# Kernel optimization log

Hardware: AMD Instinct MI355X
Metric: run time of the kernel (lower is better)

## Reference

```python
import jax, jax.numpy as jnp
import numpy as np

SCALE = 100.0          # sigmoid sharpness used as soft comparator in long division
PRECISION_BITS = 16    # number of long-division iterations (ReciprocalFFN layers)


def setup_inputs() -> dict:
    key = jax.random.key(0)
    kq, kk, kv = jax.random.split(key, 3)
    B, D, N = 8192, 1024, 2048
    return {
        "query": jax.random.normal(kq, (B, D), dtype=jnp.float32),
        "keys": jax.random.normal(kk, (N, D), dtype=jnp.float32),
        "values": jax.random.normal(kv, (N, D), dtype=jnp.float32),
    }


def _reciprocal_scan(divisor):
    """16-step non-restoring long division computing ~1/divisor.

    Mirrors ReciprocalFFN: state = (remainder, quotient), remainder starts at 1,
    each step: doubled = 2*r; step = sigmoid(SCALE*(doubled - d));
    r' = doubled - d*step; q' = q + 2^{-(i+1)} * step.
    divisor: (B, 1) -> returns quotient (B, 1).
    """
    bit_weights = 2.0 ** -(jnp.arange(PRECISION_BITS, dtype=jnp.float32) + 1.0)

    def body(carry, w):
        r, q = carry
        doubled = r * 2.0
        step = jax.nn.sigmoid(SCALE * (doubled - divisor))
        return (doubled - divisor * step, q + w * step), None

    init = (jnp.ones_like(divisor), jnp.zeros_like(divisor))
    (_, quotient), _ = jax.lax.scan(body, init, bit_weights)
    return quotient


def reference(query, keys, values):
    # Baked-mode forward: QK scores -> softmax1 with FFN long-division reciprocal
    # -> weighted sum of values.
    scale = keys.shape[-1] ** -0.5
    scores = jnp.einsum("bd,nd->bn", query, keys) * scale          # (B, N)
    exps = jnp.exp(scores - jnp.max(scores, axis=-1, keepdims=True))
    sum_exp = 1.0 + jnp.sum(exps, axis=-1, keepdims=True)           # (B, 1)
    reciprocal = _reciprocal_scan(sum_exp)                          # (B, 1)
    weights = exps * reciprocal                                     # (B, N)
    return jnp.einsum("bn,nd->bd", weights, values)                 # (B, D)
```

## Files before the change

### kernel.cpp

```cpp
#include <hip/hip_runtime.h>
#include <hip/hip_bf16.h>
#include <stdint.h>

#define BQ   8192
#define DIM  1024
#define NK   2048

typedef unsigned short u16;
using f32x4  = __attribute__((ext_vector_type(4))) float;
using bf16x8 = __attribute__((ext_vector_type(8))) __bf16;
using f16x8  = __attribute__((ext_vector_type(8))) _Float16;
using u16x4  = __attribute__((ext_vector_type(4))) unsigned short;
using u16x8  = __attribute__((ext_vector_type(8))) unsigned short;


__device__ __forceinline__ u16 f2bf(float f) {
    uint32_t u = __float_as_uint(f);
    u += 0x7FFFu + ((u >> 16) & 1u);
    return (u16)(u >> 16);
}

__device__ __forceinline__ u16 f2h(float f) {
    _Float16 h = (_Float16)f;
    return __builtin_bit_cast(unsigned short, h);
}

__device__ __forceinline__ void gload_lds16(const void* g, void* l) {
    __builtin_amdgcn_global_load_lds(
        (const __attribute__((address_space(1))) void*)g,
        (__attribute__((address_space(3))) void*)l,
        16, 0, 0);
}

template<bool F16>
__device__ __forceinline__ f32x4 mfmaT(u16x8 a, u16x8 b, f32x4 c) {
    if constexpr (F16)
        return __builtin_amdgcn_mfma_f32_16x16x32_f16(
            __builtin_bit_cast(f16x8, a), __builtin_bit_cast(f16x8, b), c, 0, 0, 0);
    else
        return __builtin_amdgcn_mfma_f32_16x16x32_bf16(
            __builtin_bit_cast(bf16x8, a), __builtin_bit_cast(bf16x8, b), c, 0, 0, 0);
}


__global__ void cvt_f32_bf16(const float* __restrict__ in, u16* __restrict__ out, int n4) {
    int i = blockIdx.x * blockDim.x + threadIdx.x;
    if (i < n4) {
        f32x4 v = reinterpret_cast<const f32x4*>(in)[i];
        u16x4 o;
        o.x = f2bf(v[0]); o.y = f2bf(v[1]); o.z = f2bf(v[2]); o.w = f2bf(v[3]);
        reinterpret_cast<u16x4*>(out)[i] = o;
    }
}

__global__ void transpose_cvt(const float* __restrict__ V, u16* __restrict__ VT) {
    __shared__ float tile[32][33];
    int d0 = blockIdx.x * 32;
    int n0 = blockIdx.y * 32;
    int tx = threadIdx.x, ty = threadIdx.y;
#pragma unroll
    for (int i = 0; i < 4; ++i)
        tile[ty + i * 8][tx] = V[(size_t)(n0 + ty + i * 8) * DIM + d0 + tx];
    __syncthreads();
#pragma unroll
    for (int i = 0; i < 4; ++i)
        VT[(size_t)(d0 + ty + i * 8) * NK + n0 + tx] = f2h(tile[tx][ty + i * 8]);
}


template<int BN, bool F16, typename OT>
__global__ __launch_bounds__(512, 2)
void gemm256(const u16* __restrict__ A, const u16* __restrict__ B, OT* __restrict__ C,
             int K, int lda, int ldb, int ldc, float scale, int nbn) {
    constexpr int WTN  = BN / 4;
    constexpr int NREP = BN / 64;
    constexpr int NH   = NREP / 2;
    constexpr int BCALLS = (BN == 256) ? 4 : 2;

    __shared__ u16 As[2][256 * 64];
    __shared__ u16 Bs[2][BN * 64];

    const int tid  = threadIdx.x;
    const int wave = tid >> 6;
    const int lane = tid & 63;
    const int wr = wave >> 2;
    const int wc = wave & 3;

    int id = blockIdx.x;
    const int cpx = gridDim.x >> 3;
    id = (id & 7) * cpx + (id >> 3);
    const int bm = id / nbn;
    const int bn = id % nbn;

    const int lsub  = lane >> 3;
    const int lslot = lane & 7;
    const int srcColEl = ((lslot ^ lsub) << 3);

    const int aRow0 = wr * 128 + wc * 32;
    int bRow0;
    if constexpr (BN == 256) bRow0 = (wc >> 1) * 128 + (wr * 2 + (wc & 1)) * 32;
    else                     bRow0 = wave * 16;

    const u16* aSrc = A + (size_t)(bm * 256 + aRow0 + lsub) * lda + srcColEl;
    const u16* bSrc = B + (size_t)(bn * BN  + bRow0 + lsub) * ldb + srcColEl;

    f32x4 acc[8][NREP] = {};

    const int NT = K >> 6;

    auto STAGE = [&](int buf, int kt) {
        const size_t ko = (size_t)kt * 64;
#pragma unroll
        for (int c2 = 0; c2 < 4; ++c2)
            gload_lds16(aSrc + (size_t)c2 * 8 * lda + ko, &As[buf][(aRow0 + c2 * 8) * 64]);
#pragma unroll
        for (int c2 = 0; c2 < BCALLS; ++c2)
            gload_lds16(bSrc + (size_t)c2 * 8 * ldb + ko, &Bs[buf][(bRow0 + c2 * 8) * 64]);
    };

    auto LDA_frag = [&](const char* base, int m, int kk) -> u16x8 {
        int r   = wr * 128 + m * 16 + (lane & 15);
        int off = r * 128 + (((kk * 64) + ((lane >> 4) << 4)) ^ ((lane & 7) << 4));
        return *reinterpret_cast<const u16x8*>(base + off);
    };
    auto LDB_frag = [&](const char* base, int n, int kk) -> u16x8 {
        int r   = wc * WTN + n * 16 + (lane & 15);
        int off = r * 128 + (((kk * 64) + ((lane >> 4) << 4)) ^ ((lane & 7) << 4));
        return *reinterpret_cast<const u16x8*>(base + off);
    };

    STAGE(0, 0);
    __syncthreads();

    int cbuf = 0;
    for (int t = 0; t < NT; ++t) {
        if (t + 1 < NT) STAGE(cbuf ^ 1, t + 1);
        __builtin_amdgcn_sched_barrier(0);

        const char* aB = (const char*)&As[cbuf][0];
        const char* bB = (const char*)&Bs[cbuf][0];

        u16x8 af[4][2];
        u16x8 bf0[NH][2], bf1[NH][2];

#pragma unroll
        for (int mi = 0; mi < 4; ++mi) { af[mi][0] = LDA_frag(aB, mi, 0); af[mi][1] = LDA_frag(aB, mi, 1); }
#pragma unroll
        for (int ni = 0; ni < NH; ++ni) { bf0[ni][0] = LDB_frag(bB, ni, 0); bf0[ni][1] = LDB_frag(bB, ni, 1); }
        __builtin_amdgcn_s_setprio(1);
#pragma unroll
        for (int mi = 0; mi < 4; ++mi)
#pragma unroll
            for (int ni = 0; ni < NH; ++ni) {
                acc[mi][ni] = mfmaT<F16>(af[mi][0], bf0[ni][0], acc[mi][ni]);
                acc[mi][ni] = mfmaT<F16>(af[mi][1], bf0[ni][1], acc[mi][ni]);
            }
        __builtin_amdgcn_s_setprio(0);

#pragma unroll
        for (int ni = 0; ni < NH; ++ni) { bf1[ni][0] = LDB_frag(bB, NH + ni, 0); bf1[ni][1] = LDB_frag(bB, NH + ni, 1); }
        __builtin_amdgcn_s_setprio(1);
#pragma unroll
        for (int mi = 0; mi < 4; ++mi)
#pragma unroll
            for (int ni = 0; ni < NH; ++ni) {
                acc[mi][NH + ni] = mfmaT<F16>(af[mi][0], bf1[ni][0], acc[mi][NH + ni]);
                acc[mi][NH + ni] = mfmaT<F16>(af[mi][1], bf1[ni][1], acc[mi][NH + ni]);
            }
        __builtin_amdgcn_s_setprio(0);

#pragma unroll
        for (int mi = 0; mi < 4; ++mi) { af[mi][0] = LDA_frag(aB, 4 + mi, 0); af[mi][1] = LDA_frag(aB, 4 + mi, 1); }
        __builtin_amdgcn_s_setprio(1);
#pragma unroll
        for (int mi = 0; mi < 4; ++mi)
#pragma unroll
            for (int ni = 0; ni < NH; ++ni) {
                acc[4 + mi][NH + ni] = mfmaT<F16>(af[mi][0], bf1[ni][0], acc[4 + mi][NH + ni]);
                acc[4 + mi][NH + ni] = mfmaT<F16>(af[mi][1], bf1[ni][1], acc[4 + mi][NH + ni]);
            }
        __builtin_amdgcn_s_setprio(0);

        __builtin_amdgcn_s_setprio(1);
#pragma unroll
        for (int mi = 0; mi < 4; ++mi)
#pragma unroll
            for (int ni = 0; ni < NH; ++ni) {
                acc[4 + mi][ni] = mfmaT<F16>(af[mi][0], bf0[ni][0], acc[4 + mi][ni]);
                acc[4 + mi][ni] = mfmaT<F16>(af[mi][1], bf0[ni][1], acc[4 + mi][ni]);
            }
        __builtin_amdgcn_s_setprio(0);

        __syncthreads();
        cbuf ^= 1;
    }

    const int col0 = bn * BN + wc * WTN + (lane & 15);
    const int row0 = bm * 256 + wr * 128 + ((lane >> 4) << 2);
#pragma unroll
    for (int m = 0; m < 8; ++m) {
#pragma unroll
        for (int j = 0; j < 4; ++j) {
            int row = row0 + m * 16 + j;
            OT* cp = C + (size_t)row * ldc + col0;
#pragma unroll
            for (int n = 0; n < NREP; ++n)
                cp[n * 16] = (OT)(acc[m][n][j] * scale);
        }
    }
}


__global__ __launch_bounds__(256)
void softmax_recip_f16(const u16* __restrict__ S, u16* __restrict__ W) {
    const int lane = threadIdx.x & 63;
    const int row  = blockIdx.x * 4 + (threadIdx.x >> 6);

    const u16x8* sp = reinterpret_cast<const u16x8*>(S + (size_t)row * NK);
    u16x8 raw[4];
#pragma unroll
    for (int j = 0; j < 4; ++j) raw[j] = sp[lane + j * 64];

    float e[32];
    float mx = -1e30f;
#pragma unroll
    for (int j = 0; j < 4; ++j)
#pragma unroll
        for (int i = 0; i < 8; ++i) {
            float f = (float)__builtin_bit_cast(_Float16, (unsigned short)raw[j][i]);
            e[j * 8 + i] = f;
            mx = fmaxf(mx, f);
        }
#pragma unroll
    for (int off = 32; off; off >>= 1) mx = fmaxf(mx, __shfl_xor(mx, off));

    float sum = 0.f;
#pragma unroll
    for (int i = 0; i < 32; ++i) { e[i] = expf(e[i] - mx); sum += e[i]; }
#pragma unroll
    for (int off = 32; off; off >>= 1) sum += __shfl_xor(sum, off);

    const float d = 1.0f + sum;

    float r = 1.0f, q = 0.0f, w = 0.5f;
#pragma unroll
    for (int i = 0; i < 16; ++i) {
        float doubled = 2.0f * r;
        float st = 1.0f / (1.0f + expf(-100.0f * (doubled - d)));
        r = doubled - d * st;
        q += w * st;
        w *= 0.5f;
    }

    u16x8* wp = reinterpret_cast<u16x8*>(W + (size_t)row * NK);
#pragma unroll
    for (int j = 0; j < 4; ++j) {
        u16x8 o;
#pragma unroll
        for (int i = 0; i < 8; ++i) o[i] = f2h(e[j * 8 + i] * q);
        wp[lane + j * 64] = o;
    }
}


extern "C" void kernel_launch(void* const* d_in, const int* in_sizes, int n_in,
                              void* d_out, int out_size, void* d_ws, size_t ws_size,
                              hipStream_t stream) {
    const float* Q = (const float*)d_in[0];
    const float* K = (const float*)d_in[1];
    const float* V = (const float*)d_in[2];
    float* out = (float*)d_out;

    char* ws = (char*)d_ws;
    u16* Qb  = (u16*)(ws);
    u16* Kb  = (u16*)(ws + (16u << 20));
    u16* VhT = (u16*)(ws + (20u << 20));
    u16* S   = (u16*)(ws + (24u << 20));
    u16* W   = (u16*)(ws + (56u << 20));

    {
        int n4 = BQ * DIM / 4;
        cvt_f32_bf16<<<(n4 + 255) / 256, 256, 0, stream>>>(Q, Qb, n4);
    }
    {
        int n4 = NK * DIM / 4;
        cvt_f32_bf16<<<(n4 + 255) / 256, 256, 0, stream>>>(K, Kb, n4);
    }
    transpose_cvt<<<dim3(DIM / 32, NK / 32), dim3(32, 8), 0, stream>>>(V, VhT);

    gemm256<256, false, _Float16><<<(BQ / 256) * (NK / 256), 512, 0, stream>>>(
        Qb, Kb, (_Float16*)S, DIM, DIM, DIM, NK, 0.03125f, NK / 256);

    softmax_recip_f16<<<BQ / 4, 256, 0, stream>>>(S, W);

    gemm256<128, true, float><<<(BQ / 256) * (DIM / 128), 512, 0, stream>>>(
        W, VhT, out, NK, NK, NK, DIM, 1.0f, DIM / 128);
}
```

Measured before the change: 111.6 us.

## Shrink GEMM tiles to 128x128 with 4 waves and merge Q/K conversion kernels

Replaces the 256-row, 8-wave GEMM with a simpler 128x128, 4-wave kernel that uses a 4x4 MFMA accumulator per wave and a plain per-k-step schedule. Both GEMMs launch more, smaller blocks, which raises block count and occupancy but lowers per-block data reuse and drops the hand-interleaved fragment loads. It also fuses the two Q and K f32-to-bf16 conversion launches into one kernel to save a launch.

```diff
diff --git a/kernel.cpp b/kernel.cpp
--- a/kernel.cpp
+++ b/kernel.cpp
@@ -43,14 +43,17 @@
 }
 
 
-__global__ void cvt_f32_bf16(const float* __restrict__ in, u16* __restrict__ out, int n4) {
+__global__ void cvt_qk(const float* __restrict__ Q, const float* __restrict__ K,
+                       u16* __restrict__ Qb, u16* __restrict__ Kb, int n4Q, int n4T) {
     int i = blockIdx.x * blockDim.x + threadIdx.x;
-    if (i < n4) {
-        f32x4 v = reinterpret_cast<const f32x4*>(in)[i];
-        u16x4 o;
-        o.x = f2bf(v[0]); o.y = f2bf(v[1]); o.z = f2bf(v[2]); o.w = f2bf(v[3]);
-        reinterpret_cast<u16x4*>(out)[i] = o;
-    }
+    if (i >= n4T) return;
+    const float* src; u16* dst; int j;
+    if (i < n4Q) { src = Q; dst = Qb; j = i; }
+    else         { src = K; dst = Kb; j = i - n4Q; }
+    f32x4 v = reinterpret_cast<const f32x4*>(src)[j];
+    u16x4 o;
+    o.x = f2bf(v[0]); o.y = f2bf(v[1]); o.z = f2bf(v[2]); o.w = f2bf(v[3]);
+    reinterpret_cast<u16x4*>(dst)[j] = o;
 }
 
 __global__ void transpose_cvt(const float* __restrict__ V, u16* __restrict__ VT) {
@@ -68,23 +71,18 @@
 }
 
 
-template<int BN, bool F16, typename OT>
-__global__ __launch_bounds__(512, 2)
-void gemm256(const u16* __restrict__ A, const u16* __restrict__ B, OT* __restrict__ C,
+template<bool F16, typename OT>
+__global__ __launch_bounds__(256, 2)
+void gemm128(const u16* __restrict__ A, const u16* __restrict__ B, OT* __restrict__ C,
              int K, int lda, int ldb, int ldc, float scale, int nbn) {
-    constexpr int WTN  = BN / 4;
-    constexpr int NREP = BN / 64;
-    constexpr int NH   = NREP / 2;
-    constexpr int BCALLS = (BN == 256) ? 4 : 2;
-
-    __shared__ u16 As[2][256 * 64];
-    __shared__ u16 Bs[2][BN * 64];
+    __shared__ u16 As[2][128 * 64];
+    __shared__ u16 Bs[2][128 * 64];
 
     const int tid  = threadIdx.x;
     const int wave = tid >> 6;
     const int lane = tid & 63;
-    const int wr = wave >> 2;
-    const int wc = wave & 3;
+    const int wr = wave >> 1;
+    const int wc = wave & 1;
 
     int id = blockIdx.x;
     const int cpx = gridDim.x >> 3;
@@ -96,38 +94,35 @@
     const int lslot = lane & 7;
     const int srcColEl = ((lslot ^ lsub) << 3);
 
-    const int aRow0 = wr * 128 + wc * 32;
-    int bRow0;
-    if constexpr (BN == 256) bRow0 = (wc >> 1) * 128 + (wr * 2 + (wc & 1)) * 32;
-    else                     bRow0 = wave * 16;
-
-    const u16* aSrc = A + (size_t)(bm * 256 + aRow0 + lsub) * lda + srcColEl;
-    const u16* bSrc = B + (size_t)(bn * BN  + bRow0 + lsub) * ldb + srcColEl;
-
-    f32x4 acc[8][NREP] = {};
-
-    const int NT = K >> 6;
+    const u16* aSrc = A + (size_t)(bm * 128 + wave * 8 + lsub) * lda + srcColEl;
+    const u16* bSrc = B + (size_t)(bn * 128 + wave * 8 + lsub) * ldb + srcColEl;
+    const int dst0 = (wave * 8) * 64;
 
     auto STAGE = [&](int buf, int kt) {
         const size_t ko = (size_t)kt * 64;
 #pragma unroll
-        for (int c2 = 0; c2 < 4; ++c2)
-            gload_lds16(aSrc + (size_t)c2 * 8 * lda + ko, &As[buf][(aRow0 + c2 * 8) * 64]);
-#pragma unroll
-        for (int c2 = 0; c2 < BCALLS; ++c2)
-            gload_lds16(bSrc + (size_t)c2 * 8 * ldb + ko, &Bs[buf][(bRow0 + c2 * 8) * 64]);
+        for (int c = 0; c < 4; ++c) {
+            gload_lds16(aSrc + (size_t)(c * 32) * lda + ko, &As[buf][dst0 + c * 32 * 64]);
+            gload_lds16(bSrc + (size_t)(c * 32) * ldb + ko, &Bs[buf][dst0 + c * 32 * 64]);
+        }
     };
 
-    auto LDA_frag = [&](const char* base, int m, int kk) -> u16x8 {
-        int r   = wr * 128 + m * 16 + (lane & 15);
-        int off = r * 128 + (((kk * 64) + ((lane >> 4) << 4)) ^ ((lane & 7) << 4));
-        return *reinterpret_cast<const u16x8*>(base + off);
+    const int fr = lane & 15;
+    auto LDA_frag = [&](int buf, int m, int kk) -> u16x8 {
+        int r   = wr * 64 + m * 16 + fr;
+        int off = r * 128 + ((kk * 64 + ((lane >> 4) << 4)) ^ ((lane & 7) << 4));
+        return *reinterpret_cast<const u16x8*>(
+            reinterpret_cast<const char*>(&As[buf][0]) + off);
     };
-    auto LDB_frag = [&](const char* base, int n, int kk) -> u16x8 {
-        int r   = wc * WTN + n * 16 + (lane & 15);
-        int off = r * 128 + (((kk * 64) + ((lane >> 4) << 4)) ^ ((lane & 7) << 4));
-        return *reinterpret_cast<const u16x8*>(base + off);
+    auto LDB_frag = [&](int buf, int n, int kk) -> u16x8 {
+        int r   = wc * 64 + n * 16 + fr;
+        int off = r * 128 + ((kk * 64 + ((lane >> 4) << 4)) ^ ((lane & 7) << 4));
+        return *reinterpret_cast<const u16x8*>(
+            reinterpret_cast<const char*>(&Bs[buf][0]) + off);
     };
+
+    f32x4 acc[4][4] = {};
+    const int NT = K >> 6;
 
     STAGE(0, 0);
     __syncthreads();
@@ -137,74 +132,36 @@
         if (t + 1 < NT) STAGE(cbuf ^ 1, t + 1);
         __builtin_amdgcn_sched_barrier(0);
 
-        const char* aB = (const char*)&As[cbuf][0];
-        const char* bB = (const char*)&Bs[cbuf][0];
-
-        u16x8 af[4][2];
-        u16x8 bf0[NH][2], bf1[NH][2];
-
-#pragma unroll
-        for (int mi = 0; mi < 4; ++mi) { af[mi][0] = LDA_frag(aB, mi, 0); af[mi][1] = LDA_frag(aB, mi, 1); }
-#pragma unroll
-        for (int ni = 0; ni < NH; ++ni) { bf0[ni][0] = LDB_frag(bB, ni, 0); bf0[ni][1] = LDB_frag(bB, ni, 1); }
-        __builtin_amdgcn_s_setprio(1);
-#pragma unroll
-        for (int mi = 0; mi < 4; ++mi)
-#pragma unroll
-            for (int ni = 0; ni < NH; ++ni) {
-                acc[mi][ni] = mfmaT<F16>(af[mi][0], bf0[ni][0], acc[mi][ni]);
-                acc[mi][ni] = mfmaT<F16>(af[mi][1], bf0[ni][1], acc[mi][ni]);
-            }
-        __builtin_amdgcn_s_setprio(0);
-
-#pragma unroll
-        for (int ni = 0; ni < NH; ++ni) { bf1[ni][0] = LDB_frag(bB, NH + ni, 0); bf1[ni][1] = LDB_frag(bB, NH + ni, 1); }
-        __builtin_amdgcn_s_setprio(1);
-#pragma unroll
-        for (int mi = 0; mi < 4; ++mi)
-#pragma unroll
-            for (int ni = 0; ni < NH; ++ni) {
-                acc[mi][NH + ni] = mfmaT<F16>(af[mi][0], bf1[ni][0], acc[mi][NH + ni]);
-                acc[mi][NH + ni] = mfmaT<F16>(af[mi][1], bf1[ni][1], acc[mi][NH + ni]);
-            }
-        __builtin_amdgcn_s_setprio(0);
-
-#pragma unroll
-        for (int mi = 0; mi < 4; ++mi) { af[mi][0] = LDA_frag(aB, 4 + mi, 0); af[mi][1] = LDA_frag(aB, 4 + mi, 1); }
-        __builtin_amdgcn_s_setprio(1);
-#pragma unroll
-        for (int mi = 0; mi < 4; ++mi)
-#pragma unroll
-            for (int ni = 0; ni < NH; ++ni) {
-                acc[4 + mi][NH + ni] = mfmaT<F16>(af[mi][0], bf1[ni][0], acc[4 + mi][NH + ni]);
-                acc[4 + mi][NH + ni] = mfmaT<F16>(af[mi][1], bf1[ni][1], acc[4 + mi][NH + ni]);
-            }
-        __builtin_amdgcn_s_setprio(0);
-
-        __builtin_amdgcn_s_setprio(1);
-#pragma unroll
-        for (int mi = 0; mi < 4; ++mi)
-#pragma unroll
-            for (int ni = 0; ni < NH; ++ni) {
-                acc[4 + mi][ni] = mfmaT<F16>(af[mi][0], bf0[ni][0], acc[4 + mi][ni]);
-                acc[4 + mi][ni] = mfmaT<F16>(af[mi][1], bf0[ni][1], acc[4 + mi][ni]);
-            }
-        __builtin_amdgcn_s_setprio(0);
+#pragma unroll
+        for (int kk = 0; kk < 2; ++kk) {
+            u16x8 af[4], bf[4];
+#pragma unroll
+            for (int m = 0; m < 4; ++m) af[m] = LDA_frag(cbuf, m, kk);
+#pragma unroll
+            for (int n = 0; n < 4; ++n) bf[n] = LDB_frag(cbuf, n, kk);
+            __builtin_amdgcn_s_setprio(1);
+#pragma unroll
+            for (int m = 0; m < 4; ++m)
+#pragma unroll
+                for (int n = 0; n < 4; ++n)
+                    acc[m][n] = mfmaT<F16>(af[m], bf[n], acc[m][n]);
+            __builtin_amdgcn_s_setprio(0);
+        }
 
         __syncthreads();
         cbuf ^= 1;
     }
 
-    const int col0 = bn * BN + wc * WTN + (lane & 15);
-    const int row0 = bm * 256 + wr * 128 + ((lane >> 4) << 2);
-#pragma unroll
-    for (int m = 0; m < 8; ++m) {
+    const int col0 = bn * 128 + wc * 64 + fr;
+    const int row0 = bm * 128 + wr * 64 + ((lane >> 4) << 2);
+#pragma unroll
+    for (int m = 0; m < 4; ++m) {
 #pragma unroll
         for (int j = 0; j < 4; ++j) {
             int row = row0 + m * 16 + j;
             OT* cp = C + (size_t)row * ldc + col0;
 #pragma unroll
-            for (int n = 0; n < NREP; ++n)
+            for (int n = 0; n < 4; ++n)
                 cp[n * 16] = (OT)(acc[m][n][j] * scale);
         }
     }
@@ -279,20 +236,17 @@
     u16* W   = (u16*)(ws + (56u << 20));
 
     {
-        int n4 = BQ * DIM / 4;
-        cvt_f32_bf16<<<(n4 + 255) / 256, 256, 0, stream>>>(Q, Qb, n4);
-    }
-    {
-        int n4 = NK * DIM / 4;
-        cvt_f32_bf16<<<(n4 + 255) / 256, 256, 0, stream>>>(K, Kb, n4);
+        int n4Q = BQ * DIM / 4;
+        int n4T = n4Q + NK * DIM / 4;
+        cvt_qk<<<(n4T + 255) / 256, 256, 0, stream>>>(Q, K, Qb, Kb, n4Q, n4T);
     }
     transpose_cvt<<<dim3(DIM / 32, NK / 32), dim3(32, 8), 0, stream>>>(V, VhT);
 
-    gemm256<256, false, _Float16><<<(BQ / 256) * (NK / 256), 512, 0, stream>>>(
-        Qb, Kb, (_Float16*)S, DIM, DIM, DIM, NK, 0.03125f, NK / 256);
+    gemm128<false, _Float16><<<(BQ / 128) * (NK / 128), 256, 0, stream>>>(
+        Qb, Kb, (_Float16*)S, DIM, DIM, DIM, NK, 0.03125f, NK / 128);
 
     softmax_recip_f16<<<BQ / 4, 256, 0, stream>>>(S, W);
 
-    gemm256<128, true, float><<<(BQ / 256) * (DIM / 128), 512, 0, stream>>>(
+    gemm128<true, float><<<(BQ / 128) * (DIM / 128), 256, 0, stream>>>(
         W, VhT, out, NK, NK, NK, DIM, 1.0f, DIM / 128);
 }
```

New measurement: 119.3 us. +7.0%, slower.
